# Optimization experiments

Hardware: AMD Instinct MI355X
Metric: run time of the kernel (lower is better)

The kernel has to match this reference:

```python
import jax, jax.numpy as jnp
import numpy as np

N_NODES = 100000
N_EDGES = 1600000
D_IN = 128
D_HID = 128
N_CLS = 2


def gcn_conv(x, edge_index, W, b):
    """PyG GCNConv: add self-loops, symmetric normalization, linear, scatter-add, bias."""
    n = x.shape[0]
    loop = jnp.arange(n, dtype=edge_index.dtype)
    src = jnp.concatenate([edge_index[0], loop])  # [E+N]
    dst = jnp.concatenate([edge_index[1], loop])
    # degree computed on destination (col) after adding self-loops
    deg = jax.ops.segment_sum(jnp.ones_like(dst, dtype=x.dtype), dst, num_segments=n)
    dinv = jnp.where(deg > 0, jax.lax.rsqrt(deg), 0.0)
    norm = dinv[src] * dinv[dst]  # [E+N]
    h = x @ W  # [N, out]
    msg = h[src] * norm[:, None]  # [E+N, out]
    out = jax.ops.segment_sum(msg, dst, num_segments=n)
    return out + b


def setup_inputs() -> dict:
    key = jax.random.key(0)
    k1, k2, k3, k4 = jax.random.split(key, 4)
    x = jax.random.normal(k1, (N_NODES, D_IN), dtype=jnp.float32)
    edge_index = jax.random.randint(k2, (2, N_EDGES), 0, N_NODES, dtype=jnp.int64)
    W1 = jax.random.normal(k3, (D_IN, D_HID), dtype=jnp.float32) * (1.0 / np.sqrt(D_IN))
    b1 = jnp.zeros((D_HID,), dtype=jnp.float32)
    W2 = jax.random.normal(k4, (D_HID, N_CLS), dtype=jnp.float32) * (1.0 / np.sqrt(D_HID))
    b2 = jnp.zeros((N_CLS,), dtype=jnp.float32)
    return {"x": x, "edge_index": edge_index, "W1": W1, "b1": b1, "W2": W2, "b2": b2}


def reference(x, edge_index, W1, b1, W2, b2):
    h = gcn_conv(x, edge_index, W1, b1)
    h = jax.nn.relu(h)
    # training=False -> dropout skipped
    out = gcn_conv(h, edge_index, W2, b2)
    return out
```

## Files before the change

### kernel.cpp

```cpp
#include <hip/hip_runtime.h>
#include <hip/hip_fp16.h>
#include <cstdint>
#include <cstddef>

#define NN 100000
#define NE 1600000
#define D 128
#define NBK 782
#define NBLK_P 200
#define EPB 8000

typedef _Float16 half8 __attribute__((ext_vector_type(8)));
typedef _Float16 half4v __attribute__((ext_vector_type(4)));
typedef float f32x4 __attribute__((ext_vector_type(4)));


__launch_bounds__(256)
__global__ void p1_count_k(const int* __restrict__ ei, unsigned* __restrict__ offs,
                           const float* __restrict__ W, _Float16* __restrict__ Wt) {
    __shared__ unsigned hist[NBK];
    int tid = threadIdx.x, b = blockIdx.x;
    for (int k = tid; k < NBK; k += 256) hist[k] = 0u;
    __syncthreads();
    int e0 = b * EPB;
    for (int i = tid * 4; i < EPB; i += 1024) {
        int4 d4 = *(const int4*)(ei + NE + e0 + i);
        atomicAdd(&hist[d4.x >> 7], 1u);
        atomicAdd(&hist[d4.y >> 7], 1u);
        atomicAdd(&hist[d4.z >> 7], 1u);
        atomicAdd(&hist[d4.w >> 7], 1u);
    }
    __syncthreads();
    for (int k = tid; k < NBK; k += 256) offs[(size_t)b * NBK + k] = hist[k];

    if (b < 64) {
        int idx = b * 256 + tid;
        int n = idx >> 7, k = idx & 127;
        Wt[idx] = (_Float16)W[k * 128 + n];
    }
}

__launch_bounds__(256)
__global__ void p2a_k(unsigned* __restrict__ offs, unsigned* __restrict__ base) {
    __shared__ unsigned sh[256];
    int t = threadIdx.x, k = blockIdx.x;
    unsigned v = (t < NBLK_P) ? offs[(size_t)t * NBK + k] : 0u;
    sh[t] = v;
    __syncthreads();
    for (int off = 1; off < 256; off <<= 1) {
        unsigned u = (t >= off) ? sh[t - off] : 0u;
        __syncthreads();
        sh[t] += u;
        __syncthreads();
    }
    if (t < NBLK_P) offs[(size_t)t * NBK + k] = sh[t] - v;
    if (t == 255) base[k] = sh[255];
}

__global__ void p2b_k(unsigned* __restrict__ base) {
    __shared__ unsigned sh[1024];
    int t = threadIdx.x;
    unsigned v = (t < NBK) ? base[t] : 0u;
    sh[t] = v;
    __syncthreads();
    for (int off = 1; off < 1024; off <<= 1) {
        unsigned u = (t >= off) ? sh[t - off] : 0u;
        __syncthreads();
        sh[t] += u;
        __syncthreads();
    }
    if (t < NBK) base[t] = sh[t] - v;
    if (t == NBK) base[NBK] = sh[NBK - 1];
}

__launch_bounds__(256)
__global__ void p3_scatter_k(const int* __restrict__ ei, const unsigned* __restrict__ offs,
                             const unsigned* __restrict__ base, unsigned* __restrict__ part) {
    __shared__ unsigned lcnt[NBK];
    int tid = threadIdx.x, b = blockIdx.x;
    for (int k = tid; k < NBK; k += 256) lcnt[k] = base[k] + offs[(size_t)b * NBK + k];
    __syncthreads();
    int e0 = b * EPB;
    for (int i = tid * 4; i < EPB; i += 1024) {
        int4 s4 = *(const int4*)(ei + e0 + i);
        int4 d4 = *(const int4*)(ei + NE + e0 + i);
        unsigned p;
        p = atomicAdd(&lcnt[d4.x >> 7], 1u); part[p] = (unsigned)s4.x | ((unsigned)(d4.x & 127) << 20);
        p = atomicAdd(&lcnt[d4.y >> 7], 1u); part[p] = (unsigned)s4.y | ((unsigned)(d4.y & 127) << 20);
        p = atomicAdd(&lcnt[d4.z >> 7], 1u); part[p] = (unsigned)s4.z | ((unsigned)(d4.z & 127) << 20);
        p = atomicAdd(&lcnt[d4.w >> 7], 1u); part[p] = (unsigned)s4.w | ((unsigned)(d4.w & 127) << 20);
    }
}

__launch_bounds__(256)
__global__ void p4_csr_k(const unsigned* __restrict__ part, const unsigned* __restrict__ base,
                         unsigned* __restrict__ rp, float* __restrict__ dinv,
                         unsigned* __restrict__ col) {
    __shared__ unsigned c[128], p[128], run[128];
    int tid = threadIdx.x, k = blockIdx.x;
    int n0 = k << 7;
    int nodes = (NN - n0 < 128) ? (NN - n0) : 128;
    unsigned e0 = base[k], e1 = base[k + 1];

    if (tid < 128) c[tid] = 0u;
    __syncthreads();
    for (unsigned e = e0 + tid; e < e1; e += 256)
        atomicAdd(&c[(part[e] >> 20) & 127], 1u);
    __syncthreads();

    unsigned myc = (tid < 128) ? c[tid] : 0u;
    if (tid < 128) p[tid] = myc;
    __syncthreads();
    for (int off = 1; off < 128; off <<= 1) {
        unsigned u = 0;
        if (tid < 128 && tid >= off) u = p[tid - off];
        __syncthreads();
        if (tid < 128) p[tid] += u;
        __syncthreads();
    }
    if (tid < 128) {
        unsigned excl = p[tid] - myc;
        run[tid] = excl;
        if (tid < nodes) {
            rp[n0 + tid] = e0 + excl;
            dinv[n0 + tid] = rsqrtf((float)(myc + 1u));
        }
    }
    if (k == 0 && tid == 0) rp[NN] = NE;
    __syncthreads();

    for (unsigned e = e0 + tid; e < e1; e += 256) {
        unsigned v = part[e];
        unsigned dlo = (v >> 20) & 127;
        unsigned pos = e0 + atomicAdd(&run[dlo], 1u);
        col[pos] = v & 0xFFFFFu;
    }
}

__launch_bounds__(256)
__global__ void gemm1_k(const float* __restrict__ x, const _Float16* __restrict__ Wt,
                        const float* __restrict__ dinv, _Float16* __restrict__ h) {
    __shared__ _Float16 wt[128 * 136];
    __shared__ _Float16 xs[128 * 72];
    int tid = threadIdx.x;
    int rb = blockIdx.x * 128;
    int w = tid >> 6, lane = tid & 63;
    int m = lane & 15, q4 = lane >> 4;

#pragma unroll
    for (int q = 0; q < 8; q++) {
        int idx = q * 256 + tid;
        int n = idx >> 4, k8 = (idx & 15) * 8;
        *(half8*)(&wt[n * 136 + k8]) = *(const half8*)(Wt + n * 128 + k8);
    }

    f32x4 acc[2][8];
#pragma unroll
    for (int rt = 0; rt < 2; rt++)
#pragma unroll
        for (int nt = 0; nt < 8; nt++) acc[rt][nt] = (f32x4){0.f, 0.f, 0.f, 0.f};

    for (int ks = 0; ks <= 64; ks += 64) {
        if (ks) __syncthreads();
#pragma unroll
        for (int q = 0; q < 8; q++) {
            int idx = q * 256 + tid;
            int row = idx >> 4;
            int c4 = (idx & 15) * 4;
            int gr = rb + row;
            float4 v = (gr < NN) ? *(const float4*)(x + (size_t)gr * 128 + ks + c4)
                                 : make_float4(0, 0, 0, 0);
            half4v hv = { (_Float16)v.x, (_Float16)v.y, (_Float16)v.z, (_Float16)v.w };
            *(half4v*)(&xs[row * 72 + c4]) = hv;
        }
        __syncthreads();

#pragma unroll
        for (int kc = 0; kc < 2; kc++) {
            half8 a0 = *(const half8*)(&xs[(w * 32 + m) * 72 + kc * 32 + q4 * 8]);
            half8 a1 = *(const half8*)(&xs[(w * 32 + 16 + m) * 72 + kc * 32 + q4 * 8]);
#pragma unroll
            for (int nt = 0; nt < 8; nt++) {
                half8 bf = *(const half8*)(&wt[(nt * 16 + m) * 136 + ks + kc * 32 + q4 * 8]);
                acc[0][nt] = __builtin_amdgcn_mfma_f32_16x16x32_f16(a0, bf, acc[0][nt], 0, 0, 0);
                acc[1][nt] = __builtin_amdgcn_mfma_f32_16x16x32_f16(a1, bf, acc[1][nt], 0, 0, 0);
            }
        }
    }

    float dv[2][4];
#pragma unroll
    for (int rt = 0; rt < 2; rt++)
#pragma unroll
        for (int r = 0; r < 4; r++) {
            int ri = rb + w * 32 + rt * 16 + q4 * 4 + r;
            dv[rt][r] = (ri < NN) ? dinv[ri] : 0.f;
        }
    __syncthreads();
#pragma unroll
    for (int rt = 0; rt < 2; rt++)
#pragma unroll
        for (int nt = 0; nt < 8; nt++)
#pragma unroll
            for (int r = 0; r < 4; r++)
                wt[(w * 32 + rt * 16 + q4 * 4 + r) * 136 + nt * 16 + m] =
                    (_Float16)(acc[rt][nt][r] * dv[rt][r]);
    __syncthreads();
#pragma unroll
    for (int q = 0; q < 8; q++) {
        int idx = q * 256 + tid;
        int row = idx >> 4;
        int c8 = (idx & 15) * 8;
        int gr = rb + row;
        if (gr < NN)
            *(half8*)(h + (size_t)gr * 128 + c8) = *(const half8*)(&wt[row * 136 + c8]);
    }
}

#define GATHER(sv, vv) \
    { unsigned s_ = __builtin_amdgcn_readfirstlane(col[sv]); \
      vv = __half22float2(hb[(size_t)(s_ * 64u + lane)]); }

__launch_bounds__(256)
__global__ void agg1_k(const _Float16* __restrict__ h, const unsigned* __restrict__ rp,
                       const unsigned* __restrict__ col, const float* __restrict__ dinv,
                       const float* __restrict__ b1, const float* __restrict__ W2,
                       float* __restrict__ z) {
    int i = (blockIdx.x * 256 + threadIdx.x) >> 6;
    int lane = threadIdx.x & 63;
    if (i >= NN) return;

    const __half2* hb = (const __half2*)h;
    float di = dinv[i];
    float2 hv = __half22float2(hb[(size_t)i * 64 + lane]);
    float ax = hv.x, ay = hv.y;

    unsigned p0 = __builtin_amdgcn_readfirstlane(rp[i]);
    unsigned p1 = __builtin_amdgcn_readfirstlane(rp[i + 1]);
    unsigned e = p0;
    for (; e + 16 <= p1; e += 16) {
        float2 v0, v1, v2, v3, v4, v5, v6, v7, v8, v9, va, vb, vc, vd, ve, vf;
        GATHER(e, v0)      GATHER(e + 1, v1)  GATHER(e + 2, v2)  GATHER(e + 3, v3)
        GATHER(e + 4, v4)  GATHER(e + 5, v5)  GATHER(e + 6, v6)  GATHER(e + 7, v7)
        GATHER(e + 8, v8)  GATHER(e + 9, v9)  GATHER(e + 10, va) GATHER(e + 11, vb)
        GATHER(e + 12, vc) GATHER(e + 13, vd) GATHER(e + 14, ve) GATHER(e + 15, vf)
        ax += ((v0.x + v1.x) + (v2.x + v3.x)) + ((v4.x + v5.x) + (v6.x + v7.x))
            + ((v8.x + v9.x) + (va.x + vb.x)) + ((vc.x + vd.x) + (ve.x + vf.x));
        ay += ((v0.y + v1.y) + (v2.y + v3.y)) + ((v4.y + v5.y) + (v6.y + v7.y))
            + ((v8.y + v9.y) + (va.y + vb.y)) + ((vc.y + vd.y) + (ve.y + vf.y));
    }
    for (; e + 4 <= p1; e += 4) {
        float2 v0, v1, v2, v3;
        GATHER(e, v0) GATHER(e + 1, v1) GATHER(e + 2, v2) GATHER(e + 3, v3)
        ax += (v0.x + v1.x) + (v2.x + v3.x);
        ay += (v0.y + v1.y) + (v2.y + v3.y);
    }
    for (; e < p1; ++e) {
        float2 v;
        GATHER(e, v)
        ax += v.x;
        ay += v.y;
    }
    ax *= di;
    ay *= di;

    float2 bv = ((const float2*)b1)[lane];
    float h0 = fmaxf(ax + bv.x, 0.f);
    float h1 = fmaxf(ay + bv.y, 0.f);

    float4 w = ((const float4*)W2)[lane];
    float pz0 = fmaf(h0, w.x, h1 * w.z);
    float pz1 = fmaf(h0, w.y, h1 * w.w);
#pragma unroll
    for (int off = 32; off > 0; off >>= 1) {
        pz0 += __shfl_down(pz0, off);
        pz1 += __shfl_down(pz1, off);
    }
    if (lane == 0) {
        float2* zp = (float2*)(z + (size_t)i * 2);
        *zp = make_float2(pz0 * di, pz1 * di);
    }
}

__launch_bounds__(256)
__global__ void agg2_k(const float* __restrict__ z, const unsigned* __restrict__ rp,
                       const unsigned* __restrict__ col, const float* __restrict__ dinv,
                       const float* __restrict__ b2, float* __restrict__ out) {
    int i = (blockIdx.x * 256 + threadIdx.x) >> 4;
    int sl = threadIdx.x & 15;
    if (i >= NN) return;

    unsigned p0 = rp[i], p1 = rp[i + 1];
    float a0 = 0.f, a1 = 0.f;
    for (unsigned e = p0 + sl; e < p1; e += 16) {
        unsigned s = col[e];
        float2 v = ((const float2*)z)[s];
        a0 += v.x;
        a1 += v.y;
    }
#pragma unroll
    for (int off = 8; off > 0; off >>= 1) {
        a0 += __shfl_down(a0, off, 16);
        a1 += __shfl_down(a1, off, 16);
    }
    if (sl == 0) {
        float di = dinv[i];
        float2 zi = ((const float2*)z)[i];
        out[(size_t)i * 2]     = (a0 + zi.x) * di + b2[0];
        out[(size_t)i * 2 + 1] = (a1 + zi.y) * di + b2[1];
    }
}

extern "C" void kernel_launch(void* const* d_in, const int* in_sizes, int n_in,
                              void* d_out, int out_size, void* d_ws, size_t ws_size,
                              hipStream_t stream) {
    const float* x  = (const float*)d_in[0];
    const int*   ei = (const int*)d_in[1];
    const float* W1 = (const float*)d_in[2];
    const float* b1 = (const float*)d_in[3];
    const float* W2 = (const float*)d_in[4];
    const float* b2 = (const float*)d_in[5];
    float* out = (float*)d_out;

    char* ws = (char*)d_ws;
    unsigned* part = (unsigned*)(ws);
    unsigned* offs = (unsigned*)(ws + 6400000);
    unsigned* base = (unsigned*)(ws + 7100000);
    _Float16* h    = (_Float16*)(ws);
    float*    z    = (float*)(ws + 25600000);
    float*    dinv = (float*)(ws + 26400000);
    unsigned* rp   = (unsigned*)(ws + 26800000);
    unsigned* col  = (unsigned*)(ws + 27200016);
    _Float16* Wt   = (_Float16*)(ws + 33600016);

    p1_count_k<<<NBLK_P, 256, 0, stream>>>(ei, offs, W1, Wt);
    p2a_k<<<NBK, 256, 0, stream>>>(offs, base);
    p2b_k<<<1, 1024, 0, stream>>>(base);
    p3_scatter_k<<<NBLK_P, 256, 0, stream>>>(ei, offs, base, part);
    p4_csr_k<<<NBK, 256, 0, stream>>>(part, base, rp, dinv, col);

    gemm1_k<<<(NN + 127) / 128, 256, 0, stream>>>(x, Wt, dinv, h);
    agg1_k<<<(NN + 3) / 4, 256, 0, stream>>>(h, rp, col, dinv, b1, W2, z);
    agg2_k<<<(NN * 16 + 255) / 256, 256, 0, stream>>>(z, rp, col, dinv, b2, out);
}
```

Before: 224.3 us.

## Split each wave into four edge groups with 16-byte row gathers in agg1

Reworks the first aggregation so each 64-lane wave handles four edges at once: each group of 16 lanes loads a full 256-byte half-precision row with 8-half vector loads, instead of the whole wave gathering one row as 4-byte half2 loads. Partial sums are combined with cross-group xor shuffles before the bias, ReLU and W2 projection, which now reduce over 16 lanes. The aim is more memory-level parallelism and wider loads in the gather. In exchange, short neighbour lists waste lanes because tail edges are masked, and per-lane register use for accumulators grows.

```diff
diff --git a/kernel.cpp b/kernel.cpp
--- a/kernel.cpp
+++ b/kernel.cpp
@@ -217,10 +217,6 @@
     }
 }
 
-#define GATHER(sv, vv) \
-    { unsigned s_ = __builtin_amdgcn_readfirstlane(col[sv]); \
-      vv = __half22float2(hb[(size_t)(s_ * 64u + lane)]); }
-
 __launch_bounds__(256)
 __global__ void agg1_k(const _Float16* __restrict__ h, const unsigned* __restrict__ rp,
                        const unsigned* __restrict__ col, const float* __restrict__ dinv,
@@ -229,52 +225,67 @@
     int i = (blockIdx.x * 256 + threadIdx.x) >> 6;
     int lane = threadIdx.x & 63;
     if (i >= NN) return;
-
-    const __half2* hb = (const __half2*)h;
-    float di = dinv[i];
-    float2 hv = __half22float2(hb[(size_t)i * 64 + lane]);
-    float ax = hv.x, ay = hv.y;
+    int g = lane >> 4;
+    int c = lane & 15;
+    const _Float16* hc = h + (size_t)c * 8;
+
+    float acc[8];
+    {
+        half8 sv = *(const half8*)(hc + (size_t)i * 128);
+        float mm = (g == 0) ? 1.f : 0.f;
+#pragma unroll
+        for (int j = 0; j < 8; j++) acc[j] = mm * (float)sv[j];
+    }
 
     unsigned p0 = __builtin_amdgcn_readfirstlane(rp[i]);
     unsigned p1 = __builtin_amdgcn_readfirstlane(rp[i + 1]);
-    unsigned e = p0;
-    for (; e + 16 <= p1; e += 16) {
-        float2 v0, v1, v2, v3, v4, v5, v6, v7, v8, v9, va, vb, vc, vd, ve, vf;
-        GATHER(e, v0)      GATHER(e + 1, v1)  GATHER(e + 2, v2)  GATHER(e + 3, v3)
-        GATHER(e + 4, v4)  GATHER(e + 5, v5)  GATHER(e + 6, v6)  GATHER(e + 7, v7)
-        GATHER(e + 8, v8)  GATHER(e + 9, v9)  GATHER(e + 10, va) GATHER(e + 11, vb)
-        GATHER(e + 12, vc) GATHER(e + 13, vd) GATHER(e + 14, ve) GATHER(e + 15, vf)
-        ax += ((v0.x + v1.x) + (v2.x + v3.x)) + ((v4.x + v5.x) + (v6.x + v7.x))
-            + ((v8.x + v9.x) + (va.x + vb.x)) + ((vc.x + vd.x) + (ve.x + vf.x));
-        ay += ((v0.y + v1.y) + (v2.y + v3.y)) + ((v4.y + v5.y) + (v6.y + v7.y))
-            + ((v8.y + v9.y) + (va.y + vb.y)) + ((vc.y + vd.y) + (ve.y + vf.y));
-    }
-    for (; e + 4 <= p1; e += 4) {
-        float2 v0, v1, v2, v3;
-        GATHER(e, v0) GATHER(e + 1, v1) GATHER(e + 2, v2) GATHER(e + 3, v3)
-        ax += (v0.x + v1.x) + (v2.x + v3.x);
-        ay += (v0.y + v1.y) + (v2.y + v3.y);
-    }
-    for (; e < p1; ++e) {
-        float2 v;
-        GATHER(e, v)
-        ax += v.x;
-        ay += v.y;
-    }
-    ax *= di;
-    ay *= di;
-
-    float2 bv = ((const float2*)b1)[lane];
-    float h0 = fmaxf(ax + bv.x, 0.f);
-    float h1 = fmaxf(ay + bv.y, 0.f);
-
-    float4 w = ((const float4*)W2)[lane];
-    float pz0 = fmaf(h0, w.x, h1 * w.z);
-    float pz1 = fmaf(h0, w.y, h1 * w.w);
-#pragma unroll
-    for (int off = 32; off > 0; off >>= 1) {
-        pz0 += __shfl_down(pz0, off);
-        pz1 += __shfl_down(pz1, off);
+    for (unsigned e = p0; e < p1; e += 16) {
+        half8 v[4];
+        float mm[4];
+#pragma unroll
+        for (int q = 0; q < 4; q++) {
+            unsigned idx = e + q * 4u + (unsigned)g;
+            bool lt = idx < p1;
+            mm[q] = lt ? 1.f : 0.f;
+            unsigned s = lt ? col[idx] : 0u;
+            v[q] = *(const half8*)(hc + (size_t)s * 128);
+        }
+#pragma unroll
+        for (int q = 0; q < 4; q++)
+#pragma unroll
+            for (int j = 0; j < 8; j++)
+                acc[j] = fmaf(mm[q], (float)v[q][j], acc[j]);
+    }
+
+#pragma unroll
+    for (int j = 0; j < 8; j++) {
+        acc[j] += __shfl_xor(acc[j], 16);
+        acc[j] += __shfl_xor(acc[j], 32);
+    }
+
+    float di = dinv[i];
+    const float4* b4 = (const float4*)b1;
+    float4 ba = b4[c * 2], bb = b4[c * 2 + 1];
+    float hh[8];
+    hh[0] = fmaxf(fmaf(acc[0], di, ba.x), 0.f);
+    hh[1] = fmaxf(fmaf(acc[1], di, ba.y), 0.f);
+    hh[2] = fmaxf(fmaf(acc[2], di, ba.z), 0.f);
+    hh[3] = fmaxf(fmaf(acc[3], di, ba.w), 0.f);
+    hh[4] = fmaxf(fmaf(acc[4], di, bb.x), 0.f);
+    hh[5] = fmaxf(fmaf(acc[5], di, bb.y), 0.f);
+    hh[6] = fmaxf(fmaf(acc[6], di, bb.z), 0.f);
+    hh[7] = fmaxf(fmaf(acc[7], di, bb.w), 0.f);
+
+    const float4* w4 = (const float4*)W2;
+    float4 w0 = w4[c * 4], w1 = w4[c * 4 + 1], w2v = w4[c * 4 + 2], w3 = w4[c * 4 + 3];
+    float pz0 = hh[0] * w0.x + hh[1] * w0.z + hh[2] * w1.x + hh[3] * w1.z
+              + hh[4] * w2v.x + hh[5] * w2v.z + hh[6] * w3.x + hh[7] * w3.z;
+    float pz1 = hh[0] * w0.y + hh[1] * w0.w + hh[2] * w1.y + hh[3] * w1.w
+              + hh[4] * w2v.y + hh[5] * w2v.w + hh[6] * w3.y + hh[7] * w3.w;
+#pragma unroll
+    for (int off = 8; off > 0; off >>= 1) {
+        pz0 += __shfl_xor(pz0, off);
+        pz1 += __shfl_xor(pz1, off);
     }
     if (lane == 0) {
         float2* zp = (float2*)(z + (size_t)i * 2);
```

Result: slower. 235.1 us (+4.8%).
